# Kernel optimization log

Measured on AMD Instinct MI355X. Metric: run time of the kernel, lower is better.

## Reference

```python
import jax, jax.numpy as jnp
import numpy as np

N, E, F_NODE, F_EDGE = 100000, 400000, 64, 16
HID, HEADS, L, G, FP = 128, 4, 4, 1024, 2048
DH = HID // HEADS
T, K = 5, 32
EPS = 1e-5
NEG_SLOPE = 0.2


def _gat(x, src, dst, ea, Wl, bl, Wr, br, We, att, bias):
    """GATv2Conv (PyG semantics, eval mode): x_l=lin_l(x_src), x_r=lin_r(x_dst),
    e = att . leaky_relu(x_l[src] + x_r[dst] + lin_edge(edge_attr)),
    alpha = segment-softmax over dst, out = scatter-sum(alpha * x_l[src]) + bias."""
    n = x.shape[0]
    xl = (x @ Wl + bl).reshape(n, HEADS, DH)
    xr = (x @ Wr + br).reshape(n, HEADS, DH)
    ee = (ea @ We).reshape(-1, HEADS, DH)
    e = jax.nn.leaky_relu(xl[src] + xr[dst] + ee, NEG_SLOPE)  # [E,H,D]
    score = jnp.einsum('ehd,hd->eh', e, att)                   # [E,H]
    m = jax.ops.segment_max(score, dst, num_segments=n)        # stable softmax
    p = jnp.exp(score - m[dst])
    denom = jax.ops.segment_sum(p, dst, num_segments=n)
    alpha = p / (denom[dst] + 1e-16)
    out = jax.ops.segment_sum(alpha[:, :, None] * xl[src], dst, num_segments=n)
    return out.reshape(n, HID) + bias


def _bn_elu(h, g, b):
    # BatchNorm over the node dimension (training-mode batch stats) + ELU
    mu = h.mean(0)
    var = h.var(0)
    return jax.nn.elu((h - mu) / jnp.sqrt(var + EPS) * g + b)


def setup_inputs() -> dict:
    key = jax.random.key(0)
    ks = jax.random.split(key, 16)
    s_in = 1.0 / np.sqrt(F_NODE)
    s_h = 1.0 / np.sqrt(HID)
    s_e = 1.0 / np.sqrt(F_EDGE)
    Lh = L - 1
    return dict(
        x=jax.random.normal(ks[0], (N, F_NODE), jnp.float32),
        edge_index=jax.random.randint(ks[1], (2, E), 0, N),
        edge_attr=jax.random.normal(ks[2], (E, F_EDGE), jnp.float32),
        batch=jnp.sort(jax.random.randint(ks[3], (N,), 0, G)),
        morgan_fp=(jax.random.uniform(ks[4], (G, FP)) < 0.1).astype(jnp.float32),
        fp_idx=jnp.arange(T * K).reshape(T, K),
        Wl0=jax.random.normal(ks[5], (F_NODE, HID)) * s_in,
        bl0=jnp.zeros((HID,)),
        Wr0=jax.random.normal(ks[6], (F_NODE, HID)) * s_in,
        br0=jnp.zeros((HID,)),
        We0=jax.random.normal(ks[7], (F_EDGE, HID)) * s_e,
        att0=jax.random.normal(ks[8], (HEADS, DH)) * s_h,
        bias0=jnp.zeros((HID,)),
        g0=jnp.ones((HID,)),
        b0=jnp.zeros((HID,)),
        Wl=jax.random.normal(ks[9], (Lh, HID, HID)) * s_h,
        bl=jnp.zeros((Lh, HID)),
        Wr=jax.random.normal(ks[10], (Lh, HID, HID)) * s_h,
        br=jnp.zeros((Lh, HID)),
        We=jax.random.normal(ks[11], (Lh, F_EDGE, HID)) * s_e,
        att=jax.random.normal(ks[12], (Lh, HEADS, DH)) * s_h,
        biasc=jnp.zeros((Lh, HID)),
        g=jnp.ones((Lh, HID)),
        b=jnp.zeros((Lh, HID)),
        tw1=jax.random.normal(ks[13], (T, HID + K, HID)) / np.sqrt(HID + K),
        tb1=jnp.zeros((T, HID)),
        tw2=jax.random.normal(ks[14], (T, HID, 1)) * s_h,
        tb2=jnp.zeros((T, 1)),
    )


def reference(x, edge_index, edge_attr, batch, morgan_fp, fp_idx,
              Wl0, bl0, Wr0, br0, We0, att0, bias0, g0, b0,
              Wl, bl, Wr, br, We, att, biasc, g, b,
              tw1, tb1, tw2, tb2):
    src, dst = edge_index[0], edge_index[1]
    h = _bn_elu(_gat(x, src, dst, edge_attr, Wl0, bl0, Wr0, br0, We0, att0, bias0), g0, b0)
    for i in range(L - 1):  # residual stacked GATv2 layers
        h = _bn_elu(_gat(h, src, dst, edge_attr, Wl[i], bl[i], Wr[i], br[i],
                         We[i], att[i], biasc[i]), g[i], b[i]) + h
    counts = jax.ops.segment_sum(jnp.ones((h.shape[0],), h.dtype), batch, num_segments=G)
    emb = jax.ops.segment_sum(h, batch, num_segments=G) / jnp.maximum(counts, 1.0)[:, None]
    outs = []
    for t in range(T):  # per-task heads on [graph_emb ; selected fp bits]
        fused = jnp.concatenate([emb, morgan_fp[:, fp_idx[t]]], axis=1)
        hm = jax.nn.relu(fused @ tw1[t] + tb1[t])
        outs.append(hm @ tw2[t] + tb2[t])
    return jnp.concatenate(outs, axis=1)  # [G, T]
```

## Files before the change

kernel.cpp:

```cpp
#include <hip/hip_runtime.h>
#include <hip/hip_bf16.h>

#define N_NODES 100000
#define N_EDGES 400000
#define F_NODE_ 64
#define F_EDGE_ 16
#define HID_ 128
#define N_GRAPH 1024
#define N_TASK 5

typedef unsigned short u16;
typedef __attribute__((ext_vector_type(8))) short frag8;
typedef __attribute__((ext_vector_type(4))) float f32x4;
typedef __attribute__((ext_vector_type(2))) float f32x2;

__device__ __forceinline__ float bu2f(u16 v){ return __uint_as_float(((unsigned)v) << 16); }
__device__ __forceinline__ float2 bp2f(unsigned u){
  return make_float2(__uint_as_float(u << 16), __uint_as_float(u & 0xFFFF0000u));
}
__device__ __forceinline__ f32x2 bp2v(unsigned u){
  f32x2 r; r.x = __uint_as_float(u << 16); r.y = __uint_as_float(u & 0xFFFF0000u); return r;
}
__device__ __forceinline__ u16 f2bu(float f){
  __hip_bfloat16 h = __float2bfloat16(f);
  return *(u16*)&h;
}
__device__ __forceinline__ unsigned packbf(float a, float b){
  return (unsigned)f2bu(a) | ((unsigned)f2bu(b) << 16);
}

struct WZ12 { const float* src[12]; u16* dst[12]; int Ks[12]; int Kd[12]; };

#define CAST_BLKS ((N_NODES*F_NODE_ + 255)/256)
#define EG256 ((N_EDGES + 255)/256)
#define GOFF_BLKS ((N_GRAPH + 1 + 255)/256)
#define WSWZ_BLKS (12*64)
__global__ __launch_bounds__(256) void k_cast_hist(const float* __restrict__ s, u16* __restrict__ d,
                                                   const int* __restrict__ ei, int* __restrict__ counts,
                                                   const int* __restrict__ batch, int* __restrict__ goff,
                                                   WZ12 p){
  int b = blockIdx.x;
  if (b < CAST_BLKS){
    int i = b*256 + threadIdx.x;
    if (i < N_NODES*F_NODE_) d[i] = f2bu(s[i]);
  } else if (b < CAST_BLKS + EG256){
    int e = (b - CAST_BLKS)*256 + threadIdx.x;
    if (e < N_EDGES) atomicAdd(&counts[ei[N_EDGES + e]], 1);
  } else if (b < CAST_BLKS + EG256 + GOFF_BLKS){
    int g = (b - CAST_BLKS - EG256)*256 + threadIdx.x;
    if (g <= N_GRAPH){
      int lo = 0, hi = N_NODES;
      while (lo < hi){
        int mid = (lo + hi) >> 1;
        if (batch[mid] < g) lo = mid + 1; else hi = mid;
      }
      goff[g] = lo;
    }
  } else {
    int bb = b - CAST_BLKS - EG256 - GOFF_BLKS;
    const int sW = bb >> 6;
    const int Kd = p.Kd[sW], Ks = p.Ks[sW];
    int i = (bb & 63)*256 + threadIdx.x;
    if (i >= Kd*128) return;
    int k = i >> 7, n = i & 127;
    float v = (k < Ks) ? p.src[sW][k*128 + n] : 0.f;
    int kk = k & 31, c = k >> 5;
    int quad = kk >> 3, j = kk & 7;
    int nt = n >> 4;
    int lane = quad*16 + (n & 15);
    p.dst[sW][(((c*8 + nt)*64) + lane)*8 + j] = f2bu(v);
  }
}

#define GEMM_GRID ((N_NODES + 127)/128)
#define EPROJ_GRID ((N_EDGES + 127)/128)
__global__ __launch_bounds__(256) void k_gemm_eproj(const u16* __restrict__ A,
                                                    const u16* __restrict__ Wzl,
                                                    const u16* __restrict__ Wzr,
                                                    const float* __restrict__ bl,
                                                    const float* __restrict__ br,
                                                    u16* __restrict__ Cl,
                                                    u16* Cr,
                                                    int M, int K,
                                                    const u16* __restrict__ ea16,
                                                    const u16* __restrict__ Wez,
                                                    u16* __restrict__ eproj){
  __shared__ u16 WS[128*128];
  const int t = threadIdx.x;
  const int b = blockIdx.x;
  if (b < 2*GEMM_GRID){
    const int which = (b >= GEMM_GRID);
    const int bx = which ? b - GEMM_GRID : b;
    const u16*   Wz   = which ? Wzr : Wzl;
    const float* bias = which ? br  : bl;
    u16*         C    = which ? Cr  : Cl;
    {
      const uint4* src = (const uint4*)Wz;
      uint4* dst = (uint4*)WS;
      const int n = (K*128) >> 3;
      for (int i = t; i < n; i += 256) dst[i] = src[i];
    }
    __syncthreads();
    const int w = t >> 6, l = t & 63;
    const int m = l & 15, quad = l >> 4;
    const int rowA0 = bx*128 + w*32 + m;
    const int rowA1 = rowA0 + 16;
    f32x4 acc[2][8];
    #pragma unroll
    for (int i=0;i<2;i++)
      #pragma unroll
      for (int j=0;j<8;j++) acc[i][j] = (f32x4){0.f,0.f,0.f,0.f};
    const int KC = K >> 5;
    for (int c = 0; c < KC; c++){
      frag8 a0 = {}, a1 = {};
      if (rowA0 < M) a0 = *(const frag8*)(A + (size_t)rowA0*K + c*32 + quad*8);
      if (rowA1 < M) a1 = *(const frag8*)(A + (size_t)rowA1*K + c*32 + quad*8);
      #pragma unroll
      for (int nt = 0; nt < 8; nt++){
        frag8 bfr = *(const frag8*)&WS[(((c*8 + nt)*64) + l)*8];
        acc[0][nt] = __builtin_amdgcn_mfma_f32_16x16x32_bf16(a0, bfr, acc[0][nt], 0,0,0);
        acc[1][nt] = __builtin_amdgcn_mfma_f32_16x16x32_bf16(a1, bfr, acc[1][nt], 0,0,0);
      }
    }
    float bcv[8];
    #pragma unroll
    for (int nt=0; nt<8; nt++) bcv[nt] = bias[nt*16 + m];
    __syncthreads();
    const int sXor = quad << 4;
    #pragma unroll
    for (int rt = 0; rt < 2; rt++){
      #pragma unroll
      for (int r = 0; r < 4; r++){
        const int row = w*32 + rt*16 + quad*4 + r;
        #pragma unroll
        for (int nt = 0; nt < 8; nt++){
          const int col = nt*16 + m;
          WS[row*128 + (col ^ sXor)] = f2bu(acc[rt][nt][r] + bcv[nt]);
        }
      }
    }
    __syncthreads();
    #pragma unroll
    for (int i = 0; i < 8; i++){
      const int idx = i*256 + t;
      const int row = idx >> 4, k16 = idx & 15;
      const int grp = (k16*8) ^ (((row>>2)&3)<<4);
      const int grow = bx*128 + row;
      if (grow < M)
        *(uint4*)(C + (size_t)grow*128 + k16*8) = *(const uint4*)&WS[row*128 + grp];
    }
  } else {
    const int bx = b - 2*GEMM_GRID;
    {
      const uint4* s4 = (const uint4*)Wez;
      uint4* d4 = (uint4*)WS;
      for (int i = t; i < 512; i += 256) d4[i] = s4[i];
    }
    __syncthreads();
    const int w = t >> 6, l = t & 63, m = l & 15, quad = l >> 4;
    const int row0 = bx*128 + w*32 + m;
    const int row1 = row0 + 16;
    f32x4 acc[2][8];
    #pragma unroll
    for (int i=0;i<2;i++)
      #pragma unroll
      for (int j=0;j<8;j++) acc[i][j] = (f32x4){0.f,0.f,0.f,0.f};
    frag8 a0 = {}, a1 = {};
    if (quad < 2){
      a0 = *(const frag8*)(ea16 + (size_t)row0*16 + quad*8);
      a1 = *(const frag8*)(ea16 + (size_t)row1*16 + quad*8);
    }
    #pragma unroll
    for (int nt = 0; nt < 8; nt++){
      frag8 bfr = *(const frag8*)&WS[(nt*64 + l)*8];
      acc[0][nt] = __builtin_amdgcn_mfma_f32_16x16x32_bf16(a0, bfr, acc[0][nt], 0,0,0);
      acc[1][nt] = __builtin_amdgcn_mfma_f32_16x16x32_bf16(a1, bfr, acc[1][nt], 0,0,0);
    }
    __syncthreads();
    const int sXor = quad << 4;
    #pragma unroll
    for (int rt = 0; rt < 2; rt++){
      #pragma unroll
      for (int r = 0; r < 4; r++){
        const int row = w*32 + rt*16 + quad*4 + r;
        #pragma unroll
        for (int nt = 0; nt < 8; nt++){
          const int col = nt*16 + m;
          WS[row*128 + (col ^ sXor)] = f2bu(acc[rt][nt][r]);
        }
      }
    }
    __syncthreads();
    #pragma unroll
    for (int i = 0; i < 8; i++){
      const int idx = i*256 + t;
      const int row = idx >> 4, k16 = idx & 15;
      const int grp = (k16*8) ^ (((row>>2)&3)<<4);
      *(uint4*)(eproj + ((size_t)(bx*128 + row))*128 + k16*8) = *(const uint4*)&WS[row*128 + grp];
    }
  }
}

__global__ __launch_bounds__(512) void k_scan1(const int* __restrict__ counts,
                                               int* __restrict__ incl,
                                               int* __restrict__ bsum){
  __shared__ int s[512];
  const int t = threadIdx.x;
  int i = blockIdx.x*512 + t;
  int v = (i < N_NODES) ? counts[i] : 0;
  s[t] = v;
  __syncthreads();
  for (int off = 1; off < 512; off <<= 1){
    int x = (t >= off) ? s[t - off] : 0;
    __syncthreads();
    s[t] += x;
    __syncthreads();
  }
  if (i < N_NODES) incl[i] = s[t];
  if (t == 511) bsum[blockIdx.x] = s[511];
}

__global__ __launch_bounds__(512) void k_scan3(const int* __restrict__ counts,
                                               const int* __restrict__ incl,
                                               const int* __restrict__ bsum, int nb,
                                               int* __restrict__ offsets,
                                               int* __restrict__ cursor){
  __shared__ int sb[256];
  const int t = threadIdx.x;
  if (t < 256) sb[t] = (t < nb) ? bsum[t] : 0;
  __syncthreads();
  for (int off = 1; off < 256; off <<= 1){
    int x = 0;
    if (t < 256 && t >= off) x = sb[t - off];
    __syncthreads();
    if (t < 256) sb[t] += x;
    __syncthreads();
  }
  int i = blockIdx.x*512 + t;
  if (i >= N_NODES) return;
  int pre = (blockIdx.x == 0) ? 0 : sb[blockIdx.x - 1];
  int o = pre + incl[i];
  offsets[i + 1] = o;
  cursor[i]      = o - counts[i];
  if (i == 0) offsets[0] = 0;
}

__global__ __launch_bounds__(256) void k_scatter(const int* __restrict__ ei,
                                                 int* __restrict__ cursor,
                                                 int* __restrict__ ssrc,
                                                 const float* __restrict__ ea,
                                                 u16* __restrict__ ea16){
  int e = blockIdx.x*256 + threadIdx.x;
  if (e >= N_EDGES) return;
  int dst = ei[N_EDGES + e];
  int pos = atomicAdd(&cursor[dst], 1);
  ssrc[pos] = ei[e];
  const float* s = ea + (size_t)e*F_EDGE_;
  unsigned p[8];
  #pragma unroll
  for (int k=0;k<8;k++) p[k] = packbf(s[2*k], s[2*k+1]);
  uint4* d4 = (uint4*)(ea16 + (size_t)pos*16);
  d4[0] = make_uint4(p[0],p[1],p[2],p[3]);
  d4[1] = make_uint4(p[4],p[5],p[6],p[7]);
}

#define GAT_TILES (N_NODES/16)
#define GAT_BLOCKS ((GAT_TILES + 3)/4)
__global__ __launch_bounds__(256) void k_gat_ep(const u16* __restrict__ xl,
                                                unsigned* xr_aggr,
                                                const u16* __restrict__ eproj,
                                                const float* __restrict__ att,
                                                const int* __restrict__ offsets,
                                                const int* __restrict__ ssrc,
                                                float* __restrict__ stats){
  __shared__ float red[8][264];
  const int t = threadIdx.x;
  const int wave = t >> 6, lane = t & 63;
  const int half = lane >> 5, l32 = lane & 31;
  const int c0 = l32*4;
  const float4 av = *(const float4*)(att + c0);
  float ss0=0.f, ss1=0.f, ss2=0.f, ss3=0.f;
  float qq0=0.f, qq1=0.f, qq2=0.f, qq3=0.f;

  for (int j = 0; j < 4; j++){
    const int tile = blockIdx.x*4 + j;
    if (tile >= GAT_TILES) break;
    for (int k = 0; k < 2; k++){
      const int node = tile*16 + wave*4 + k*2 + half;
      const uint2 xru = *(const uint2*)(xr_aggr + (size_t)node*64 + l32*2);
      const f32x2 xr0 = bp2v(xru.x), xr1 = bp2v(xru.y);
      f32x2 acc0 = {0.f,0.f}, acc1 = {0.f,0.f};
      float den = 0.f;
      const int beg = offsets[node], end = offsets[node+1];
      int it = (end - beg + 3) >> 2;
      int oit = __shfl_xor(it, 32);
      const int maxit = it > oit ? it : oit;
      int i = beg;
      for (int n = 0; n < maxit; n++, i += 4){
        const int mm = end - i;
        int ib = (mm > 0) ? i : beg;
        ib = ib < N_EDGES ? ib : N_EDGES - 1;
        const int i0 = ib;
        const int i1 = (mm > 1) ? i+1 : ib;
        const int i2 = (mm > 2) ? i+2 : ib;
        const int i3 = (mm > 3) ? i+3 : ib;
        const int s0 = ssrc[i0], s1 = ssrc[i1], s2 = ssrc[i2], s3 = ssrc[i3];
        const uint2 e0 = *(const uint2*)(eproj + (size_t)i0*128 + c0);
        const uint2 e1 = *(const uint2*)(eproj + (size_t)i1*128 + c0);
        const uint2 e2 = *(const uint2*)(eproj + (size_t)i2*128 + c0);
        const uint2 e3 = *(const uint2*)(eproj + (size_t)i3*128 + c0);
        const uint2 x0 = *(const uint2*)(xl + (size_t)s0*HID_ + c0);
        const uint2 x1 = *(const uint2*)(xl + (size_t)s1*HID_ + c0);
        const uint2 x2 = *(const uint2*)(xl + (size_t)s2*HID_ + c0);
        const uint2 x3 = *(const uint2*)(xl + (size_t)s3*HID_ + c0);
        const f32x2 vl00 = bp2v(x0.x), vl01 = bp2v(x0.y);
        const f32x2 vl10 = bp2v(x1.x), vl11 = bp2v(x1.y);
        const f32x2 vl20 = bp2v(x2.x), vl21 = bp2v(x2.y);
        const f32x2 vl30 = bp2v(x3.x), vl31 = bp2v(x3.y);
        f32x2 v00 = vl00 + xr0 + bp2v(e0.x), v01 = vl01 + xr1 + bp2v(e0.y);
        f32x2 v10 = vl10 + xr0 + bp2v(e1.x), v11 = vl11 + xr1 + bp2v(e1.y);
        f32x2 v20 = vl20 + xr0 + bp2v(e2.x), v21 = vl21 + xr1 + bp2v(e2.y);
        f32x2 v30 = vl30 + xr0 + bp2v(e3.x), v31 = vl31 + xr1 + bp2v(e3.y);
        f32x2 w;
        w = v00*0.2f; v00.x = fmaxf(v00.x,w.x); v00.y = fmaxf(v00.y,w.y);
        w = v01*0.2f; v01.x = fmaxf(v01.x,w.x); v01.y = fmaxf(v01.y,w.y);
        w = v10*0.2f; v10.x = fmaxf(v10.x,w.x); v10.y = fmaxf(v10.y,w.y);
        w = v11*0.2f; v11.x = fmaxf(v11.x,w.x); v11.y = fmaxf(v11.y,w.y);
        w = v20*0.2f; v20.x = fmaxf(v20.x,w.x); v20.y = fmaxf(v20.y,w.y);
        w = v21*0.2f; v21.x = fmaxf(v21.x,w.x); v21.y = fmaxf(v21.y,w.y);
        w = v30*0.2f; v30.x = fmaxf(v30.x,w.x); v30.y = fmaxf(v30.y,w.y);
        w = v31*0.2f; v31.x = fmaxf(v31.x,w.x); v31.y = fmaxf(v31.y,w.y);
        float sc0 = v00.x*av.x + v00.y*av.y + v01.x*av.z + v01.y*av.w;
        float sc1 = v10.x*av.x + v10.y*av.y + v11.x*av.z + v11.y*av.w;
        float sc2 = v20.x*av.x + v20.y*av.y + v21.x*av.z + v21.y*av.w;
        float sc3 = v30.x*av.x + v30.y*av.y + v31.x*av.z + v31.y*av.w;
        sc0 += __shfl_xor(sc0, 1); sc1 += __shfl_xor(sc1, 1); sc2 += __shfl_xor(sc2, 1); sc3 += __shfl_xor(sc3, 1);
        sc0 += __shfl_xor(sc0, 2); sc1 += __shfl_xor(sc1, 2); sc2 += __shfl_xor(sc2, 2); sc3 += __shfl_xor(sc3, 2);
        sc0 += __shfl_xor(sc0, 4); sc1 += __shfl_xor(sc1, 4); sc2 += __shfl_xor(sc2, 4); sc3 += __shfl_xor(sc3, 4);
        const float p0 = (mm > 0) ? __expf(sc0) : 0.f;
        const float p1 = (mm > 1) ? __expf(sc1) : 0.f;
        const float p2 = (mm > 2) ? __expf(sc2) : 0.f;
        const float p3 = (mm > 3) ? __expf(sc3) : 0.f;
        acc0 += p0*vl00 + p1*vl10 + p2*vl20 + p3*vl30;
        acc1 += p0*vl01 + p1*vl11 + p2*vl21 + p3*vl31;
        den  += p0 + p1 + p2 + p3;
      }
      const float inv = 1.0f / (den + 1e-16f);
      uint2 outv;
      outv.x = packbf(acc0.x*inv, acc0.y*inv);
      outv.y = packbf(acc1.x*inv, acc1.y*inv);
      *(uint2*)(xr_aggr + (size_t)node*64 + l32*2) = outv;
      const float2 o0 = bp2f(outv.x), o1 = bp2f(outv.y);
      ss0 += o0.x; ss1 += o0.y; ss2 += o1.x; ss3 += o1.y;
      qq0 += o0.x*o0.x; qq1 += o0.y*o0.y; qq2 += o1.x*o1.x; qq3 += o1.y*o1.y;
    }
  }
  const int g = wave*2 + half;
  red[g][c0+0] = ss0; red[g][c0+1] = ss1; red[g][c0+2] = ss2; red[g][c0+3] = ss3;
  red[g][128+c0+0] = qq0; red[g][128+c0+1] = qq1; red[g][128+c0+2] = qq2; red[g][128+c0+3] = qq3;
  __syncthreads();
  {
    float a = 0.f;
    #pragma unroll
    for (int gg = 0; gg < 8; gg++) a += red[gg][t];
    atomicAdd(&stats[t], a);
  }
}

__global__ __launch_bounds__(256) void k_bn_apply(const unsigned* __restrict__ aggr_b,
                                                  const float* __restrict__ stats,
                                                  const float* __restrict__ gamma,
                                                  const float* __restrict__ beta,
                                                  u16* __restrict__ h, int residual){
  size_t i = (size_t)blockIdx.x*256 + threadIdx.x;
  if (i >= (size_t)N_NODES*16) return;
  const int c = (int)((i & 15) * 8);
  const float invn = 1.0f / (float)N_NODES;
  uint4 v4 = ((const uint4*)aggr_b)[i];
  uint4* hp = (uint4*)h + i;
  uint4 hv4 = make_uint4(0,0,0,0);
  if (residual) hv4 = *hp;
  unsigned vin[4]  = {v4.x, v4.y, v4.z, v4.w};
  unsigned hin[4]  = {hv4.x, hv4.y, hv4.z, hv4.w};
  unsigned outw[4];
  #pragma unroll
  for (int j=0;j<4;j++){
    int cc = c + j*2;
    float mu0  = stats[cc]   * invn,  mu1  = stats[cc+1]   * invn;
    float var0 = stats[128+cc]*invn - mu0*mu0;
    float var1 = stats[129+cc]*invn - mu1*mu1;
    float sc0 = rsqrtf(var0 + 1e-5f) * gamma[cc];
    float sc1 = rsqrtf(var1 + 1e-5f) * gamma[cc+1];
    float2 v = bp2f(vin[j]);
    float val0 = (v.x - mu0) * sc0 + beta[cc];
    float val1 = (v.y - mu1) * sc1 + beta[cc+1];
    val0 = val0 > 0.f ? val0 : expm1f(val0);
    val1 = val1 > 0.f ? val1 : expm1f(val1);
    if (residual){
      float2 hv = bp2f(hin[j]);
      val0 += hv.x; val1 += hv.y;
    }
    outw[j] = packbf(val0, val1);
  }
  *hp = make_uint4(outw[0], outw[1], outw[2], outw[3]);
}

__global__ __launch_bounds__(256) void k_pool_seg(const unsigned* __restrict__ h2,
                                                  const int* __restrict__ goff,
                                                  float* __restrict__ emb){
  __shared__ float redS[4][128];
  const int g = blockIdx.x, t = threadIdx.x;
  const int p = t & 63, rg = t >> 6;
  const int beg = goff[g], end = goff[g+1];
  float a0 = 0.f, a1 = 0.f;
  for (int r = beg + rg; r < end; r += 4){
    float2 v = bp2f(h2[(size_t)r*64 + p]);
    a0 += v.x; a1 += v.y;
  }
  redS[rg][p*2] = a0; redS[rg][p*2+1] = a1;
  __syncthreads();
  if (rg == 0){
    #pragma unroll
    for (int k=1;k<4;k++){ a0 += redS[k][p*2]; a1 += redS[k][p*2+1]; }
    float n = fmaxf((float)(end - beg), 1.f);
    emb[(size_t)g*HID_ + p*2]     = a0 / n;
    emb[(size_t)g*HID_ + p*2 + 1] = a1 / n;
  }
}

#define HG 8
__global__ __launch_bounds__(128) void k_heads(const float* __restrict__ emb,
                                               const float* __restrict__ mf,
                                               const int* __restrict__ fpi,
                                               const float* __restrict__ tw1,
                                               const float* __restrict__ tb1,
                                               const float* __restrict__ tw2,
                                               const float* __restrict__ tb2,
                                               float* __restrict__ out){
  const int task = blockIdx.y, g0 = blockIdx.x*HG;
  const int j = threadIdx.x;
  __shared__ float fused[HG][160];
  __shared__ float red[HG][128];
  for (int idx = j; idx < HG*160; idx += 128){
    int g = idx / 160, i = idx % 160;
    float v;
    if (i < 128) v = emb[(size_t)(g0+g)*HID_ + i];
    else         v = mf[(size_t)(g0+g)*2048 + fpi[task*32 + (i-128)]];
    fused[g][i] = v;
  }
  __syncthreads();
  const float* w1 = tw1 + (size_t)task*160*128;
  float acc[HG];
  float b1 = tb1[task*128 + j];
  #pragma unroll
  for (int g=0; g<HG; g++) acc[g] = b1;
  for (int i=0; i<160; i++){
    float wv = w1[(size_t)i*128 + j];
    #pragma unroll
    for (int g=0; g<HG; g++) acc[g] += fused[g][i] * wv;
  }
  float t2 = tw2[task*128 + j];
  #pragma unroll
  for (int g=0; g<HG; g++){
    float v = acc[g] > 0.f ? acc[g] : 0.f;
    red[g][j] = v * t2;
  }
  __syncthreads();
  int g = j >> 4, l16 = j & 15;
  float s = 0.f;
  #pragma unroll
  for (int k=0;k<8;k++) s += red[g][l16 + k*16];
  s += __shfl_xor(s, 1, 16);
  s += __shfl_xor(s, 2, 16);
  s += __shfl_xor(s, 4, 16);
  s += __shfl_xor(s, 8, 16);
  if (l16 == 0) out[(size_t)(g0+g)*N_TASK + task] = s + tb2[task];
}

extern "C" void kernel_launch(void* const* d_in, const int* in_sizes, int n_in,
                              void* d_out, int out_size, void* d_ws, size_t ws_size,
                              hipStream_t stream){
  const float* x    = (const float*)d_in[0];
  const int*   ei   = (const int*)  d_in[1];
  const float* ea   = (const float*)d_in[2];
  const int*   batch= (const int*)  d_in[3];
  const float* mf   = (const float*)d_in[4];
  const int*   fpi  = (const int*)  d_in[5];
  const float* Wl0  = (const float*)d_in[6];
  const float* bl0  = (const float*)d_in[7];
  const float* Wr0  = (const float*)d_in[8];
  const float* br0  = (const float*)d_in[9];
  const float* We0  = (const float*)d_in[10];
  const float* att0 = (const float*)d_in[11];
  const float* g0   = (const float*)d_in[13];
  const float* b0   = (const float*)d_in[14];
  const float* Wl   = (const float*)d_in[15];
  const float* bl   = (const float*)d_in[16];
  const float* Wr   = (const float*)d_in[17];
  const float* br   = (const float*)d_in[18];
  const float* We   = (const float*)d_in[19];
  const float* att  = (const float*)d_in[20];
  const float* gg   = (const float*)d_in[22];
  const float* bb   = (const float*)d_in[23];
  const float* tw1  = (const float*)d_in[24];
  const float* tb1  = (const float*)d_in[25];
  const float* tw2  = (const float*)d_in[26];
  const float* tb2  = (const float*)d_in[27];
  float* out = (float*)d_out;

  char* w = (char*)d_ws;
  auto alloc = [&](size_t bytes)->char*{ char* r = w; w += (bytes + 255) & ~(size_t)255; return r; };
  u16*   xl     = (u16*)  alloc((size_t)N_NODES*HID_*2);
  unsigned* xr_aggr = (unsigned*)alloc((size_t)N_NODES*64*4);
  u16*   h      = (u16*)  alloc((size_t)N_NODES*HID_*2);
  u16*   ea16   = (u16*)  alloc((size_t)N_EDGES*16*2);
  int*   counts = (int*)  alloc((size_t)N_NODES*4);
  float* stats4 = (float*)alloc(4*256*4);
  int*   offsets= (int*)  alloc((size_t)(N_NODES+1)*4);
  int*   cursor = (int*)  alloc((size_t)N_NODES*4);
  int*   incl   = (int*)  alloc((size_t)N_NODES*4);
  int*   bsum   = (int*)  alloc(256*4);
  int*   ssrc   = (int*)  alloc((size_t)N_EDGES*4);
  int*   goff   = (int*)  alloc((size_t)(N_GRAPH+1)*4);
  float* emb    = (float*)alloc((size_t)N_GRAPH*HID_*4);
  u16*   Wzl0   = (u16*)  alloc((size_t)F_NODE_*128*2);
  u16*   Wzr0   = (u16*)  alloc((size_t)F_NODE_*128*2);
  u16*   Wzl123 = (u16*)  alloc((size_t)3*HID_*128*2);
  u16*   Wzr123 = (u16*)  alloc((size_t)3*HID_*128*2);
  u16*   Wez4   = (u16*)  alloc((size_t)4*32*128*2);
  u16*   eproj  = (u16*)  alloc((size_t)N_EDGES*HID_*2);
  u16*   xbf    = (u16*)  alloc((size_t)N_NODES*F_NODE_*2);

  const size_t zlen = (size_t)((char*)(stats4 + 4*256) - (char*)counts);
  const int nscan = (N_NODES + 511)/512;

  WZ12 p;
  p.src[0] = Wl0; p.dst[0] = Wzl0; p.Ks[0] = F_NODE_; p.Kd[0] = F_NODE_;
  p.src[1] = Wr0; p.dst[1] = Wzr0; p.Ks[1] = F_NODE_; p.Kd[1] = F_NODE_;
  for (int i=0;i<3;i++){
    p.src[2+i] = Wl + (size_t)i*HID_*HID_; p.dst[2+i] = Wzl123 + (size_t)i*HID_*128; p.Ks[2+i] = HID_; p.Kd[2+i] = HID_;
    p.src[5+i] = Wr + (size_t)i*HID_*HID_; p.dst[5+i] = Wzr123 + (size_t)i*HID_*128; p.Ks[5+i] = HID_; p.Kd[5+i] = HID_;
  }
  p.src[8] = We0; p.dst[8] = Wez4; p.Ks[8] = F_EDGE_; p.Kd[8] = 32;
  for (int i=0;i<3;i++){
    p.src[9+i] = We + (size_t)i*F_EDGE_*HID_; p.dst[9+i] = Wez4 + (size_t)(i+1)*32*128; p.Ks[9+i] = F_EDGE_; p.Kd[9+i] = 32;
  }

  hipMemsetAsync(counts, 0, zlen, stream);
  hipLaunchKernelGGL(k_cast_hist, dim3(CAST_BLKS + EG256 + GOFF_BLKS + WSWZ_BLKS), dim3(256), 0, stream,
                     x, xbf, ei, counts, batch, goff, p);
  hipLaunchKernelGGL(k_scan1,  dim3(nscan), dim3(512), 0, stream, counts, incl, bsum);
  hipLaunchKernelGGL(k_scan3,  dim3(nscan), dim3(512), 0, stream, counts, incl, bsum, nscan, offsets, cursor);
  hipLaunchKernelGGL(k_scatter,dim3(EG256), dim3(256), 0, stream, ei, cursor, ssrc, ea, ea16);

  for (int layer = 0; layer < 4; layer++){
    const float *bl_, *br_, *att_, *g_, *b_;
    const u16 *Wzl_, *Wzr_, *Ain;
    int K;
    if (layer == 0){
      bl_=bl0; br_=br0; att_=att0; g_=g0; b_=b0;
      Wzl_ = Wzl0; Wzr_ = Wzr0; Ain = xbf; K = F_NODE_;
    } else {
      int i = layer - 1;
      bl_ = bl + (size_t)i*HID_;  br_ = br + (size_t)i*HID_;
      att_= att + (size_t)i*HID_;
      g_  = gg + (size_t)i*HID_;  b_  = bb + (size_t)i*HID_;
      Wzl_ = Wzl123 + (size_t)i*HID_*128;
      Wzr_ = Wzr123 + (size_t)i*HID_*128;
      Ain = h; K = HID_;
    }
    float* stats = stats4 + layer*256;
    hipLaunchKernelGGL(k_gemm_eproj, dim3(2*GEMM_GRID + EPROJ_GRID), dim3(256), 0, stream,
                       Ain, Wzl_, Wzr_, bl_, br_, xl, (u16*)xr_aggr, N_NODES, K,
                       ea16, Wez4 + (size_t)layer*32*128, eproj);
    hipLaunchKernelGGL(k_gat_ep, dim3(GAT_BLOCKS), dim3(256), 0, stream,
                       xl, xr_aggr, eproj, att_, offsets, ssrc, stats);
    hipLaunchKernelGGL(k_bn_apply, dim3((N_NODES*16 + 255)/256), dim3(256), 0, stream,
                       xr_aggr, stats, g_, b_, h, layer > 0 ? 1 : 0);
  }
  hipLaunchKernelGGL(k_pool_seg, dim3(N_GRAPH), dim3(256), 0, stream, (const unsigned*)h, goff, emb);
  hipLaunchKernelGGL(k_heads, dim3(N_GRAPH/HG, N_TASK), dim3(128), 0, stream, emb, mf, fpi, tw1, tb1, tw2, tb2, out);
}
```

Measured before the change: 761.6 us.

## Shrink GAT blocks, stripe BN stat atomics, precompute BN affine, fuse pool+heads

The GAT edge kernel now uses 128-thread blocks covering 8 nodes each, giving a much larger grid, in place of 256-thread blocks that loop over 64 nodes. BN statistics are accumulated into 8 striped copies to cut atomic contention, and the BN apply kernel folds mean, variance, gamma and beta into a per-channel scale and shift in shared memory once per block. Mean pooling and the task heads are fused into one kernel, which removes a launch and the emb round trip but gives fewer blocks for the heads work.

```diff
diff --git a/kernel.cpp b/kernel.cpp
--- a/kernel.cpp
+++ b/kernel.cpp
@@ -264,16 +264,15 @@
   d4[1] = make_uint4(p[4],p[5],p[6],p[7]);
 }
 
-#define GAT_TILES (N_NODES/16)
-#define GAT_BLOCKS ((GAT_TILES + 3)/4)
-__global__ __launch_bounds__(256) void k_gat_ep(const u16* __restrict__ xl,
+#define GAT_GRID (N_NODES/8)
+__global__ __launch_bounds__(128) void k_gat_ep(const u16* __restrict__ xl,
                                                 unsigned* xr_aggr,
                                                 const u16* __restrict__ eproj,
                                                 const float* __restrict__ att,
                                                 const int* __restrict__ offsets,
                                                 const int* __restrict__ ssrc,
                                                 float* __restrict__ stats){
-  __shared__ float red[8][264];
+  __shared__ float red[4][264];
   const int t = threadIdx.x;
   const int wave = t >> 6, lane = t & 63;
   const int half = lane >> 5, l32 = lane & 31;
@@ -282,88 +281,86 @@
   float ss0=0.f, ss1=0.f, ss2=0.f, ss3=0.f;
   float qq0=0.f, qq1=0.f, qq2=0.f, qq3=0.f;
 
-  for (int j = 0; j < 4; j++){
-    const int tile = blockIdx.x*4 + j;
-    if (tile >= GAT_TILES) break;
-    for (int k = 0; k < 2; k++){
-      const int node = tile*16 + wave*4 + k*2 + half;
-      const uint2 xru = *(const uint2*)(xr_aggr + (size_t)node*64 + l32*2);
-      const f32x2 xr0 = bp2v(xru.x), xr1 = bp2v(xru.y);
-      f32x2 acc0 = {0.f,0.f}, acc1 = {0.f,0.f};
-      float den = 0.f;
-      const int beg = offsets[node], end = offsets[node+1];
-      int it = (end - beg + 3) >> 2;
-      int oit = __shfl_xor(it, 32);
-      const int maxit = it > oit ? it : oit;
-      int i = beg;
-      for (int n = 0; n < maxit; n++, i += 4){
-        const int mm = end - i;
-        int ib = (mm > 0) ? i : beg;
-        ib = ib < N_EDGES ? ib : N_EDGES - 1;
-        const int i0 = ib;
-        const int i1 = (mm > 1) ? i+1 : ib;
-        const int i2 = (mm > 2) ? i+2 : ib;
-        const int i3 = (mm > 3) ? i+3 : ib;
-        const int s0 = ssrc[i0], s1 = ssrc[i1], s2 = ssrc[i2], s3 = ssrc[i3];
-        const uint2 e0 = *(const uint2*)(eproj + (size_t)i0*128 + c0);
-        const uint2 e1 = *(const uint2*)(eproj + (size_t)i1*128 + c0);
-        const uint2 e2 = *(const uint2*)(eproj + (size_t)i2*128 + c0);
-        const uint2 e3 = *(const uint2*)(eproj + (size_t)i3*128 + c0);
-        const uint2 x0 = *(const uint2*)(xl + (size_t)s0*HID_ + c0);
-        const uint2 x1 = *(const uint2*)(xl + (size_t)s1*HID_ + c0);
-        const uint2 x2 = *(const uint2*)(xl + (size_t)s2*HID_ + c0);
-        const uint2 x3 = *(const uint2*)(xl + (size_t)s3*HID_ + c0);
-        const f32x2 vl00 = bp2v(x0.x), vl01 = bp2v(x0.y);
-        const f32x2 vl10 = bp2v(x1.x), vl11 = bp2v(x1.y);
-        const f32x2 vl20 = bp2v(x2.x), vl21 = bp2v(x2.y);
-        const f32x2 vl30 = bp2v(x3.x), vl31 = bp2v(x3.y);
-        f32x2 v00 = vl00 + xr0 + bp2v(e0.x), v01 = vl01 + xr1 + bp2v(e0.y);
-        f32x2 v10 = vl10 + xr0 + bp2v(e1.x), v11 = vl11 + xr1 + bp2v(e1.y);
-        f32x2 v20 = vl20 + xr0 + bp2v(e2.x), v21 = vl21 + xr1 + bp2v(e2.y);
-        f32x2 v30 = vl30 + xr0 + bp2v(e3.x), v31 = vl31 + xr1 + bp2v(e3.y);
-        f32x2 w;
-        w = v00*0.2f; v00.x = fmaxf(v00.x,w.x); v00.y = fmaxf(v00.y,w.y);
-        w = v01*0.2f; v01.x = fmaxf(v01.x,w.x); v01.y = fmaxf(v01.y,w.y);
-        w = v10*0.2f; v10.x = fmaxf(v10.x,w.x); v10.y = fmaxf(v10.y,w.y);
-        w = v11*0.2f; v11.x = fmaxf(v11.x,w.x); v11.y = fmaxf(v11.y,w.y);
-        w = v20*0.2f; v20.x = fmaxf(v20.x,w.x); v20.y = fmaxf(v20.y,w.y);
-        w = v21*0.2f; v21.x = fmaxf(v21.x,w.x); v21.y = fmaxf(v21.y,w.y);
-        w = v30*0.2f; v30.x = fmaxf(v30.x,w.x); v30.y = fmaxf(v30.y,w.y);
-        w = v31*0.2f; v31.x = fmaxf(v31.x,w.x); v31.y = fmaxf(v31.y,w.y);
-        float sc0 = v00.x*av.x + v00.y*av.y + v01.x*av.z + v01.y*av.w;
-        float sc1 = v10.x*av.x + v10.y*av.y + v11.x*av.z + v11.y*av.w;
-        float sc2 = v20.x*av.x + v20.y*av.y + v21.x*av.z + v21.y*av.w;
-        float sc3 = v30.x*av.x + v30.y*av.y + v31.x*av.z + v31.y*av.w;
-        sc0 += __shfl_xor(sc0, 1); sc1 += __shfl_xor(sc1, 1); sc2 += __shfl_xor(sc2, 1); sc3 += __shfl_xor(sc3, 1);
-        sc0 += __shfl_xor(sc0, 2); sc1 += __shfl_xor(sc1, 2); sc2 += __shfl_xor(sc2, 2); sc3 += __shfl_xor(sc3, 2);
-        sc0 += __shfl_xor(sc0, 4); sc1 += __shfl_xor(sc1, 4); sc2 += __shfl_xor(sc2, 4); sc3 += __shfl_xor(sc3, 4);
-        const float p0 = (mm > 0) ? __expf(sc0) : 0.f;
-        const float p1 = (mm > 1) ? __expf(sc1) : 0.f;
-        const float p2 = (mm > 2) ? __expf(sc2) : 0.f;
-        const float p3 = (mm > 3) ? __expf(sc3) : 0.f;
-        acc0 += p0*vl00 + p1*vl10 + p2*vl20 + p3*vl30;
-        acc1 += p0*vl01 + p1*vl11 + p2*vl21 + p3*vl31;
-        den  += p0 + p1 + p2 + p3;
-      }
-      const float inv = 1.0f / (den + 1e-16f);
-      uint2 outv;
-      outv.x = packbf(acc0.x*inv, acc0.y*inv);
-      outv.y = packbf(acc1.x*inv, acc1.y*inv);
-      *(uint2*)(xr_aggr + (size_t)node*64 + l32*2) = outv;
-      const float2 o0 = bp2f(outv.x), o1 = bp2f(outv.y);
-      ss0 += o0.x; ss1 += o0.y; ss2 += o1.x; ss3 += o1.y;
-      qq0 += o0.x*o0.x; qq1 += o0.y*o0.y; qq2 += o1.x*o1.x; qq3 += o1.y*o1.y;
-    }
+  for (int k = 0; k < 2; k++){
+    const int node = blockIdx.x*8 + wave*4 + k*2 + half;
+    const uint2 xru = *(const uint2*)(xr_aggr + (size_t)node*64 + l32*2);
+    const f32x2 xr0 = bp2v(xru.x), xr1 = bp2v(xru.y);
+    f32x2 acc0 = {0.f,0.f}, acc1 = {0.f,0.f};
+    float den = 0.f;
+    const int beg = offsets[node], end = offsets[node+1];
+    int it = (end - beg + 3) >> 2;
+    int oit = __shfl_xor(it, 32);
+    const int maxit = it > oit ? it : oit;
+    int i = beg;
+    for (int n = 0; n < maxit; n++, i += 4){
+      const int mm = end - i;
+      int ib = (mm > 0) ? i : beg;
+      ib = ib < N_EDGES ? ib : N_EDGES - 1;
+      const int i0 = ib;
+      const int i1 = (mm > 1) ? i+1 : ib;
+      const int i2 = (mm > 2) ? i+2 : ib;
+      const int i3 = (mm > 3) ? i+3 : ib;
+      const int s0 = ssrc[i0], s1 = ssrc[i1], s2 = ssrc[i2], s3 = ssrc[i3];
+      const uint2 e0 = *(const uint2*)(eproj + (size_t)i0*128 + c0);
+      const uint2 e1 = *(const uint2*)(eproj + (size_t)i1*128 + c0);
+      const uint2 e2 = *(const uint2*)(eproj + (size_t)i2*128 + c0);
+      const uint2 e3 = *(const uint2*)(eproj + (size_t)i3*128 + c0);
+      const uint2 x0 = *(const uint2*)(xl + (size_t)s0*HID_ + c0);
+      const uint2 x1 = *(const uint2*)(xl + (size_t)s1*HID_ + c0);
+      const uint2 x2 = *(const uint2*)(xl + (size_t)s2*HID_ + c0);
+      const uint2 x3 = *(const uint2*)(xl + (size_t)s3*HID_ + c0);
+      const f32x2 vl00 = bp2v(x0.x), vl01 = bp2v(x0.y);
+      const f32x2 vl10 = bp2v(x1.x), vl11 = bp2v(x1.y);
+      const f32x2 vl20 = bp2v(x2.x), vl21 = bp2v(x2.y);
+      const f32x2 vl30 = bp2v(x3.x), vl31 = bp2v(x3.y);
+      f32x2 v00 = vl00 + xr0 + bp2v(e0.x), v01 = vl01 + xr1 + bp2v(e0.y);
+      f32x2 v10 = vl10 + xr0 + bp2v(e1.x), v11 = vl11 + xr1 + bp2v(e1.y);
+      f32x2 v20 = vl20 + xr0 + bp2v(e2.x), v21 = vl21 + xr1 + bp2v(e2.y);
+      f32x2 v30 = vl30 + xr0 + bp2v(e3.x), v31 = vl31 + xr1 + bp2v(e3.y);
+      f32x2 w;
+      w = v00*0.2f; v00.x = fmaxf(v00.x,w.x); v00.y = fmaxf(v00.y,w.y);
+      w = v01*0.2f; v01.x = fmaxf(v01.x,w.x); v01.y = fmaxf(v01.y,w.y);
+      w = v10*0.2f; v10.x = fmaxf(v10.x,w.x); v10.y = fmaxf(v10.y,w.y);
+      w = v11*0.2f; v11.x = fmaxf(v11.x,w.x); v11.y = fmaxf(v11.y,w.y);
+      w = v20*0.2f; v20.x = fmaxf(v20.x,w.x); v20.y = fmaxf(v20.y,w.y);
+      w = v21*0.2f; v21.x = fmaxf(v21.x,w.x); v21.y = fmaxf(v21.y,w.y);
+      w = v30*0.2f; v30.x = fmaxf(v30.x,w.x); v30.y = fmaxf(v30.y,w.y);
+      w = v31*0.2f; v31.x = fmaxf(v31.x,w.x); v31.y = fmaxf(v31.y,w.y);
+      float sc0 = v00.x*av.x + v00.y*av.y + v01.x*av.z + v01.y*av.w;
+      float sc1 = v10.x*av.x + v10.y*av.y + v11.x*av.z + v11.y*av.w;
+      float sc2 = v20.x*av.x + v20.y*av.y + v21.x*av.z + v21.y*av.w;
+      float sc3 = v30.x*av.x + v30.y*av.y + v31.x*av.z + v31.y*av.w;
+      sc0 += __shfl_xor(sc0, 1); sc1 += __shfl_xor(sc1, 1); sc2 += __shfl_xor(sc2, 1); sc3 += __shfl_xor(sc3, 1);
+      sc0 += __shfl_xor(sc0, 2); sc1 += __shfl_xor(sc1, 2); sc2 += __shfl_xor(sc2, 2); sc3 += __shfl_xor(sc3, 2);
+      sc0 += __shfl_xor(sc0, 4); sc1 += __shfl_xor(sc1, 4); sc2 += __shfl_xor(sc2, 4); sc3 += __shfl_xor(sc3, 4);
+      const float p0 = (mm > 0) ? __expf(sc0) : 0.f;
+      const float p1 = (mm > 1) ? __expf(sc1) : 0.f;
+      const float p2 = (mm > 2) ? __expf(sc2) : 0.f;
+      const float p3 = (mm > 3) ? __expf(sc3) : 0.f;
+      acc0 += p0*vl00 + p1*vl10 + p2*vl20 + p3*vl30;
+      acc1 += p0*vl01 + p1*vl11 + p2*vl21 + p3*vl31;
+      den  += p0 + p1 + p2 + p3;
+    }
+    const float inv = 1.0f / (den + 1e-16f);
+    uint2 outv;
+    outv.x = packbf(acc0.x*inv, acc0.y*inv);
+    outv.y = packbf(acc1.x*inv, acc1.y*inv);
+    *(uint2*)(xr_aggr + (size_t)node*64 + l32*2) = outv;
+    const float2 o0 = bp2f(outv.x), o1 = bp2f(outv.y);
+    ss0 += o0.x; ss1 += o0.y; ss2 += o1.x; ss3 += o1.y;
+    qq0 += o0.x*o0.x; qq1 += o0.y*o0.y; qq2 += o1.x*o1.x; qq3 += o1.y*o1.y;
   }
   const int g = wave*2 + half;
   red[g][c0+0] = ss0; red[g][c0+1] = ss1; red[g][c0+2] = ss2; red[g][c0+3] = ss3;
   red[g][128+c0+0] = qq0; red[g][128+c0+1] = qq1; red[g][128+c0+2] = qq2; red[g][128+c0+3] = qq3;
   __syncthreads();
   {
-    float a = 0.f;
-    #pragma unroll
-    for (int gg = 0; gg < 8; gg++) a += red[gg][t];
-    atomicAdd(&stats[t], a);
+    float a = 0.f, b2 = 0.f;
+    #pragma unroll
+    for (int gg = 0; gg < 4; gg++){ a += red[gg][t]; b2 += red[gg][128+t]; }
+    const int base = (blockIdx.x & 7)*256;
+    atomicAdd(&stats[base + t],       a);
+    atomicAdd(&stats[base + 128 + t], b2);
   }
 }
 
@@ -372,10 +369,26 @@
                                                   const float* __restrict__ gamma,
                                                   const float* __restrict__ beta,
                                                   u16* __restrict__ h, int residual){
-  size_t i = (size_t)blockIdx.x*256 + threadIdx.x;
+  __shared__ float sc_sh[128], sh_sh[128];
+  const int t = threadIdx.x;
+  if (t < 128){
+    float s = 0.f, q = 0.f;
+    #pragma unroll
+    for (int st = 0; st < 8; st++){
+      s += stats[st*256 + t];
+      q += stats[st*256 + 128 + t];
+    }
+    const float invn = 1.0f / (float)N_NODES;
+    float mu = s * invn;
+    float var = q * invn - mu*mu;
+    float sc = rsqrtf(var + 1e-5f) * gamma[t];
+    sc_sh[t] = sc;
+    sh_sh[t] = beta[t] - mu * sc;
+  }
+  __syncthreads();
+  size_t i = (size_t)blockIdx.x*256 + t;
   if (i >= (size_t)N_NODES*16) return;
   const int c = (int)((i & 15) * 8);
-  const float invn = 1.0f / (float)N_NODES;
   uint4 v4 = ((const uint4*)aggr_b)[i];
   uint4* hp = (uint4*)h + i;
   uint4 hv4 = make_uint4(0,0,0,0);
@@ -386,14 +399,9 @@
   #pragma unroll
   for (int j=0;j<4;j++){
     int cc = c + j*2;
-    float mu0  = stats[cc]   * invn,  mu1  = stats[cc+1]   * invn;
-    float var0 = stats[128+cc]*invn - mu0*mu0;
-    float var1 = stats[129+cc]*invn - mu1*mu1;
-    float sc0 = rsqrtf(var0 + 1e-5f) * gamma[cc];
-    float sc1 = rsqrtf(var1 + 1e-5f) * gamma[cc+1];
     float2 v = bp2f(vin[j]);
-    float val0 = (v.x - mu0) * sc0 + beta[cc];
-    float val1 = (v.y - mu1) * sc1 + beta[cc+1];
+    float val0 = v.x * sc_sh[cc]   + sh_sh[cc];
+    float val1 = v.y * sc_sh[cc+1] + sh_sh[cc+1];
     val0 = val0 > 0.f ? val0 : expm1f(val0);
     val1 = val1 > 0.f ? val1 : expm1f(val1);
     if (residual){
@@ -405,76 +413,83 @@
   *hp = make_uint4(outw[0], outw[1], outw[2], outw[3]);
 }
 
-__global__ __launch_bounds__(256) void k_pool_seg(const unsigned* __restrict__ h2,
-                                                  const int* __restrict__ goff,
-                                                  float* __restrict__ emb){
+#define HG 8
+__global__ __launch_bounds__(256) void k_pool_heads(const unsigned* __restrict__ h2,
+                                                    const int* __restrict__ goff,
+                                                    const float* __restrict__ mf,
+                                                    const int* __restrict__ fpi,
+                                                    const float* __restrict__ tw1,
+                                                    const float* __restrict__ tb1,
+                                                    const float* __restrict__ tw2,
+                                                    const float* __restrict__ tb2,
+                                                    float* __restrict__ out){
+  __shared__ float emb_sh[HG][128];
+  __shared__ float fp_sh[HG][32];
+  __shared__ float red[HG][128];
   __shared__ float redS[4][128];
-  const int g = blockIdx.x, t = threadIdx.x;
+  const int t = threadIdx.x;
+  const int g0 = blockIdx.x*HG;
   const int p = t & 63, rg = t >> 6;
-  const int beg = goff[g], end = goff[g+1];
-  float a0 = 0.f, a1 = 0.f;
-  for (int r = beg + rg; r < end; r += 4){
-    float2 v = bp2f(h2[(size_t)r*64 + p]);
-    a0 += v.x; a1 += v.y;
-  }
-  redS[rg][p*2] = a0; redS[rg][p*2+1] = a1;
-  __syncthreads();
-  if (rg == 0){
-    #pragma unroll
-    for (int k=1;k<4;k++){ a0 += redS[k][p*2]; a1 += redS[k][p*2+1]; }
-    float n = fmaxf((float)(end - beg), 1.f);
-    emb[(size_t)g*HID_ + p*2]     = a0 / n;
-    emb[(size_t)g*HID_ + p*2 + 1] = a1 / n;
-  }
-}
-
-#define HG 8
-__global__ __launch_bounds__(128) void k_heads(const float* __restrict__ emb,
-                                               const float* __restrict__ mf,
-                                               const int* __restrict__ fpi,
-                                               const float* __restrict__ tw1,
-                                               const float* __restrict__ tb1,
-                                               const float* __restrict__ tw2,
-                                               const float* __restrict__ tb2,
-                                               float* __restrict__ out){
-  const int task = blockIdx.y, g0 = blockIdx.x*HG;
-  const int j = threadIdx.x;
-  __shared__ float fused[HG][160];
-  __shared__ float red[HG][128];
-  for (int idx = j; idx < HG*160; idx += 128){
-    int g = idx / 160, i = idx % 160;
-    float v;
-    if (i < 128) v = emb[(size_t)(g0+g)*HID_ + i];
-    else         v = mf[(size_t)(g0+g)*2048 + fpi[task*32 + (i-128)]];
-    fused[g][i] = v;
-  }
-  __syncthreads();
-  const float* w1 = tw1 + (size_t)task*160*128;
-  float acc[HG];
-  float b1 = tb1[task*128 + j];
-  #pragma unroll
-  for (int g=0; g<HG; g++) acc[g] = b1;
-  for (int i=0; i<160; i++){
-    float wv = w1[(size_t)i*128 + j];
-    #pragma unroll
-    for (int g=0; g<HG; g++) acc[g] += fused[g][i] * wv;
-  }
-  float t2 = tw2[task*128 + j];
-  #pragma unroll
-  for (int g=0; g<HG; g++){
-    float v = acc[g] > 0.f ? acc[g] : 0.f;
-    red[g][j] = v * t2;
-  }
-  __syncthreads();
-  int g = j >> 4, l16 = j & 15;
-  float s = 0.f;
-  #pragma unroll
-  for (int k=0;k<8;k++) s += red[g][l16 + k*16];
-  s += __shfl_xor(s, 1, 16);
-  s += __shfl_xor(s, 2, 16);
-  s += __shfl_xor(s, 4, 16);
-  s += __shfl_xor(s, 8, 16);
-  if (l16 == 0) out[(size_t)(g0+g)*N_TASK + task] = s + tb2[task];
+  for (int gl = 0; gl < HG; gl++){
+    const int beg = goff[g0+gl], end = goff[g0+gl+1];
+    float a0 = 0.f, a1 = 0.f;
+    for (int r = beg + rg; r < end; r += 4){
+      float2 v = bp2f(h2[(size_t)r*64 + p]);
+      a0 += v.x; a1 += v.y;
+    }
+    redS[rg][p*2] = a0; redS[rg][p*2+1] = a1;
+    __syncthreads();
+    if (rg == 0){
+      #pragma unroll
+      for (int k=1;k<4;k++){ a0 += redS[k][p*2]; a1 += redS[k][p*2+1]; }
+      float n = fmaxf((float)(end - beg), 1.f);
+      emb_sh[gl][p*2]     = a0 / n;
+      emb_sh[gl][p*2 + 1] = a1 / n;
+    }
+    __syncthreads();
+  }
+  const int th = t >> 7, j = t & 127;
+  for (int task = 0; task < N_TASK; task++){
+    {
+      int g = t >> 5, i = t & 31;
+      fp_sh[g][i] = mf[(size_t)(g0+g)*2048 + fpi[task*32 + i]];
+    }
+    __syncthreads();
+    const float* w1 = tw1 + (size_t)task*160*128;
+    float acc[4];
+    float b1 = tb1[task*128 + j];
+    #pragma unroll
+    for (int g=0;g<4;g++) acc[g] = b1;
+    for (int i=0;i<128;i++){
+      float wv = w1[(size_t)i*128 + j];
+      #pragma unroll
+      for (int g=0;g<4;g++) acc[g] += emb_sh[th*4+g][i] * wv;
+    }
+    for (int i=0;i<32;i++){
+      float wv = w1[(size_t)(128+i)*128 + j];
+      #pragma unroll
+      for (int g=0;g<4;g++) acc[g] += fp_sh[th*4+g][i] * wv;
+    }
+    float t2 = tw2[task*128 + j];
+    #pragma unroll
+    for (int g=0;g<4;g++){
+      float v = acc[g] > 0.f ? acc[g] : 0.f;
+      red[th*4+g][j] = v * t2;
+    }
+    __syncthreads();
+    if (t < 128){
+      int g = t >> 4, l16 = t & 15;
+      float s = 0.f;
+      #pragma unroll
+      for (int k=0;k<8;k++) s += red[g][l16 + k*16];
+      s += __shfl_xor(s, 1, 16);
+      s += __shfl_xor(s, 2, 16);
+      s += __shfl_xor(s, 4, 16);
+      s += __shfl_xor(s, 8, 16);
+      if (l16 == 0) out[(size_t)(g0+g)*N_TASK + task] = s + tb2[task];
+    }
+    __syncthreads();
+  }
 }
 
 extern "C" void kernel_launch(void* const* d_in, const int* in_sizes, int n_in,
@@ -515,7 +530,7 @@
   u16*   h      = (u16*)  alloc((size_t)N_NODES*HID_*2);
   u16*   ea16   = (u16*)  alloc((size_t)N_EDGES*16*2);
   int*   counts = (int*)  alloc((size_t)N_NODES*4);
-  float* stats4 = (float*)alloc(4*256*4);
+  float* stats4 = (float*)alloc(4*2048*4);
   int*   offsets= (int*)  alloc((size_t)(N_NODES+1)*4);
   int*   cursor = (int*)  alloc((size_t)N_NODES*4);
   int*   incl   = (int*)  alloc((size_t)N_NODES*4);
@@ -531,7 +546,7 @@
   u16*   eproj  = (u16*)  alloc((size_t)N_EDGES*HID_*2);
   u16*   xbf    = (u16*)  alloc((size_t)N_NODES*F_NODE_*2);
 
-  const size_t zlen = (size_t)((char*)(stats4 + 4*256) - (char*)counts);
+  const size_t zlen = (size_t)((char*)(stats4 + 4*2048) - (char*)counts);
   const int nscan = (N_NODES + 511)/512;
 
   WZ12 p;
@@ -569,15 +584,15 @@
       Wzr_ = Wzr123 + (size_t)i*HID_*128;
       Ain = h; K = HID_;
     }
-    float* stats = stats4 + layer*256;
+    float* stats = stats4 + layer*2048;
     hipLaunchKernelGGL(k_gemm_eproj, dim3(2*GEMM_GRID + EPROJ_GRID), dim3(256), 0, stream,
                        Ain, Wzl_, Wzr_, bl_, br_, xl, (u16*)xr_aggr, N_NODES, K,
                        ea16, Wez4 + (size_t)layer*32*128, eproj);
-    hipLaunchKernelGGL(k_gat_ep, dim3(GAT_BLOCKS), dim3(256), 0, stream,
+    hipLaunchKernelGGL(k_gat_ep, dim3(GAT_GRID), dim3(128), 0, stream,
                        xl, xr_aggr, eproj, att_, offsets, ssrc, stats);
     hipLaunchKernelGGL(k_bn_apply, dim3((N_NODES*16 + 255)/256), dim3(256), 0, stream,
                        xr_aggr, stats, g_, b_, h, layer > 0 ? 1 : 0);
   }
-  hipLaunchKernelGGL(k_pool_seg, dim3(N_GRAPH), dim3(256), 0, stream, (const unsigned*)h, goff, emb);
-  hipLaunchKernelGGL(k_heads, dim3(N_GRAPH/HG, N_TASK), dim3(128), 0, stream, emb, mf, fpi, tw1, tb1, tw2, tb2, out);
-}
+  hipLaunchKernelGGL(k_pool_heads, dim3(N_GRAPH/HG), dim3(256), 0, stream,
+                     (const unsigned*)h, goff, mf, fpi, tw1, tb1, tw2, tb2, out);
+}
```

Result: faster. 730.2 us (-4.1%).
